# Kernel tuning notes

Hardware: AMD Instinct MI355X
Metric: run time of the kernel (lower is better)

## Reference

```python
import jax, jax.numpy as jnp
import numpy as np

B, P, O, C = 64, 8732, 32, 81
IMG = 224.0
THRESH = 0.5
NEG_POS = 3.0
ALPHA = 1.0


def cxcy_to_xy(b):
    return jnp.concatenate([b[..., :2] - b[..., 2:] / 2, b[..., :2] + b[..., 2:] / 2], -1)


def xy_to_cxcy(b):
    return jnp.concatenate([(b[..., :2] + b[..., 2:]) / 2, b[..., 2:] - b[..., :2]], -1)


def coco_to_xy(b):  # [x, y, w, h] -> [xmin, ymin, xmax, ymax]
    return jnp.concatenate([b[..., :2], b[..., :2] + b[..., 2:]], -1)


def cxcy_to_gcxgcy(cxcy, priors):  # SSD offset encoding, variances 10 / 5
    g_cxcy = (cxcy[..., :2] - priors[..., :2]) / (priors[..., 2:] / 10.0)
    g_wh = jnp.log(cxcy[..., 2:] / priors[..., 2:]) * 5.0
    return jnp.concatenate([g_cxcy, g_wh], -1)


def pairwise_iou(a, b):  # a: [O,4] xy, b: [P,4] xy -> [O,P]
    lt = jnp.maximum(a[:, None, :2], b[None, :, :2])
    rb = jnp.minimum(a[:, None, 2:], b[None, :, 2:])
    wh = jnp.clip(rb - lt, 0.0)
    inter = wh[..., 0] * wh[..., 1]
    area_a = (a[:, 2] - a[:, 0]) * (a[:, 3] - a[:, 1])
    area_b = (b[:, 2] - b[:, 0]) * (b[:, 3] - b[:, 1])
    return inter / (area_a[:, None] + area_b[None, :] - inter)


def setup_inputs() -> dict:
    key = jax.random.key(0)
    k1, k2, k3, k4, k5, k6, k7 = jax.random.split(key, 7)
    pred_locs = jax.random.normal(k1, (B, P, 4), dtype=jnp.float32)
    pred_scores = jax.random.normal(k2, (B, P, C), dtype=jnp.float32)
    # COCO-format gt boxes [x, y, w, h] in pixel coords, guaranteed inside image
    xy = jax.random.uniform(k3, (B, O, 2), minval=0.0, maxval=IMG * 0.55)
    wh = jax.random.uniform(k4, (B, O, 2), minval=8.0, maxval=IMG * 0.4)
    gt_boxes = jnp.concatenate([xy, wh], -1)
    gt_labels = jax.random.randint(k5, (B, O), 1, C)  # foreground labels 1..C-1
    p_cxcy = jax.random.uniform(k6, (P, 2), minval=0.05, maxval=0.95)
    p_wh = jax.random.uniform(k7, (P, 2), minval=0.05, maxval=0.5)
    priors_cxcy = jnp.concatenate([p_cxcy, p_wh], -1)
    return {"pred_locs": pred_locs, "pred_scores": pred_scores,
            "gt_boxes": gt_boxes, "gt_labels": gt_labels,
            "priors_cxcy": priors_cxcy}


def reference(pred_locs, pred_scores, gt_boxes, gt_labels, priors_cxcy):
    priors_xy = cxcy_to_xy(priors_cxcy)

    def match(boxes_coco, labels):  # one image: [O,4] coco, [O] int
        boxes_xy = coco_to_xy(boxes_coco) / IMG  # normalize to [0,1]
        ov = pairwise_iou(boxes_xy, priors_xy)  # [O, P]
        overlap_for_prior = ov.max(axis=0)       # [P]
        object_for_prior = ov.argmax(axis=0)     # [P]
        prior_for_object = ov.argmax(axis=1)     # [O]
        # force each object to claim its best prior
        object_for_prior = object_for_prior.at[prior_for_object].set(jnp.arange(O))
        overlap_for_prior = overlap_for_prior.at[prior_for_object].set(1.0)
        label_for_prior = labels[object_for_prior]
        label_for_prior = jnp.where(overlap_for_prior < THRESH, 0, label_for_prior)
        true_locs = cxcy_to_gcxgcy(xy_to_cxcy(boxes_xy[object_for_prior]), priors_cxcy)
        return true_locs, label_for_prior

    true_locs, true_classes = jax.vmap(match)(gt_boxes, gt_labels)  # [B,P,4], [B,P]

    positive = true_classes != 0          # [B, P]
    n_pos = positive.sum(axis=1)          # [B]
    n_pos_cl = jnp.maximum(n_pos, 1).astype(jnp.float32)
    n_hard_neg = NEG_POS * n_pos_cl

    # SmoothL1 (beta=1), mean over positive prior coords
    diff = jnp.abs(pred_locs - true_locs)
    sl1 = jnp.where(diff < 1.0, 0.5 * diff * diff, diff - 0.5)  # [B,P,4]
    total_pos = n_pos.sum()
    loc_loss = jnp.where(
        total_pos > 0,
        jnp.where(positive[..., None], sl1, 0.0).sum()
        / jnp.maximum(total_pos * 4, 1).astype(jnp.float32),
        0.0,
    )

    # per-prior cross entropy
    logp = jax.nn.log_softmax(pred_scores, axis=-1)
    ce = -jnp.take_along_axis(logp, true_classes[..., None], axis=-1)[..., 0]  # [B,P]

    conf_pos_sum = jnp.where(positive, ce, 0.0).sum()
    ce_neg = jnp.where(positive, 0.0, ce)
    ce_neg_sorted = -jnp.sort(-ce_neg, axis=1)  # descending per image
    ranks = jnp.arange(P)[None, :]
    hard = ranks < n_hard_neg[:, None]
    conf_hard_neg_sum = jnp.where(hard, ce_neg_sorted, 0.0).sum()

    conf_loss = (conf_hard_neg_sum + conf_pos_sum) / n_pos_cl.sum()
    return conf_loss + ALPHA * loc_loss
```

## Files before the change

### kernel.cpp

```cpp
#include <hip/hip_runtime.h>
#include <cstdint>
#include <cstddef>

#define BB 64
#define PP 8732
#define OO 32
#define CC 81
#define NR 64
#define NB3 137
#define NQ 4
#define QP 2183

__global__ __launch_bounds__(1024) void k_prep(
    const float* __restrict__ gt_boxes,
    const float4* __restrict__ priors,
    unsigned long long* __restrict__ part,
    int* __restrict__ done)
{
    int q = blockIdx.x, b = blockIdx.y, t = threadIdx.x;
    if (q == 0 && b == 0 && t == 0) *done = 0;
    int o = t >> 5, s = t & 31;
    __shared__ float4 s_pr[1024];
    const float* g = gt_boxes + ((size_t)b * OO + o) * 4;
    float x1 = g[0] / 224.0f, y1 = g[1] / 224.0f;
    float x2 = (g[0] + g[2]) / 224.0f, y2 = (g[1] + g[3]) / 224.0f;
    float area = (x2 - x1) * (y2 - y1);
    float best = -1.0f; int bp = 0;
    int p0 = q * QP;
    for (int base = 0; base < QP; base += 1024) {
        int idx = base + t;
        if (idx < QP) s_pr[t] = priors[p0 + idx];
        __syncthreads();
        int lim = QP - base; if (lim > 1024) lim = 1024;
        for (int j = s; j < lim; j += 128) {
            float iou4[4]; int jj4[4];
            #pragma unroll
            for (int u = 0; u < 4; ++u) {
                int jj = j + 32 * u;
                jj4[u] = jj;
                if (jj < lim) {
                    float4 pr = s_pr[jj];
                    float px1 = pr.x - pr.z * 0.5f, py1 = pr.y - pr.w * 0.5f;
                    float px2 = pr.x + pr.z * 0.5f, py2 = pr.y + pr.w * 0.5f;
                    float parea = (px2 - px1) * (py2 - py1);
                    float lx = fmaxf(x1, px1), ly = fmaxf(y1, py1);
                    float rx = fminf(x2, px2), ry = fminf(y2, py2);
                    float w = fmaxf(rx - lx, 0.0f), h = fmaxf(ry - ly, 0.0f);
                    float inter = w * h;
                    iou4[u] = inter / (area + parea - inter);
                } else iou4[u] = -2.0f;
            }
            #pragma unroll
            for (int u = 0; u < 4; ++u)
                if (iou4[u] > best) { best = iou4[u]; bp = p0 + base + jj4[u]; }
        }
        __syncthreads();
    }
    unsigned long long v = ((unsigned long long)__float_as_uint(best) << 32)
                         | (unsigned long long)(0xFFFFFFFFu - (unsigned)bp);
    #pragma unroll
    for (int sh = 16; sh >= 1; sh >>= 1) {
        unsigned long long u = __shfl_xor(v, sh, 32);
        if (u > v) v = u;
    }
    if (s == 0) part[((size_t)b * NQ + q) * OO + o] = v;
}

__global__ __launch_bounds__(256) void k_ce(
    const float* __restrict__ scores,
    const float4* __restrict__ pred_locs,
    const float* __restrict__ gt_boxes,
    const int* __restrict__ gt_labels,
    const float4* __restrict__ priors,
    const unsigned long long* __restrict__ part,
    float* __restrict__ ceneg,
    float* __restrict__ pp_posce, float* __restrict__ pp_sl1,
    int* __restrict__ pp_np)
{
    int b = blockIdx.y, tid = threadIdx.x;
    int row0 = blockIdx.x * NR;
    int nrows = PP - row0; if (nrows > NR) nrows = NR;

    __shared__ float sv[NR * CC];
    __shared__ float4 s_pr[NR];
    __shared__ float bx1[OO], by1[OO], bx2[OO], by2[OO], bar[OO];
    __shared__ int s_lab[OO];
    __shared__ int s_pfo[OO];
    __shared__ int s_force[NR];
    __shared__ float s_cn[NR];
    __shared__ float s_posce, s_sl1;
    __shared__ int s_np;

    if (tid == 0) { s_posce = 0.f; s_sl1 = 0.f; s_np = 0; }
    if (tid < OO) {
        const float* g = gt_boxes + ((size_t)b * OO + tid) * 4;
        float x1 = g[0] / 224.0f, y1 = g[1] / 224.0f;
        float x2 = (g[0] + g[2]) / 224.0f, y2 = (g[1] + g[3]) / 224.0f;
        bx1[tid] = x1; by1[tid] = y1; bx2[tid] = x2; by2[tid] = y2;
        bar[tid] = (x2 - x1) * (y2 - y1);
        s_lab[tid] = gt_labels[b * OO + tid];
        const unsigned long long* pb = part + (size_t)b * NQ * OO + tid;
        unsigned long long m = pb[0];
        #pragma unroll
        for (int qq = 1; qq < NQ; ++qq) {
            unsigned long long v = pb[qq * OO];
            if (v > m) m = v;
        }
        s_pfo[tid] = (int)(0xFFFFFFFFu - (unsigned)(m & 0xFFFFFFFFull));
    }
    if (tid < NR) {
        s_force[tid] = -1;
        if (row0 + tid < PP) s_pr[tid] = priors[row0 + tid];
    }
    __syncthreads();
    if (tid == 0) {
        #pragma unroll
        for (int o = 0; o < OO; ++o) {
            int rp = s_pfo[o] - row0;
            if (rp >= 0 && rp < nrows) s_force[rp] = o;
        }
    }
    {
        const float4* src4 = (const float4*)(scores + ((size_t)b * PP + row0) * CC);
        int nvec = nrows * CC / 4;
        float4* dst = (float4*)sv;
        for (int i = tid; i < nvec; i += 256) dst[i] = src4[i];
    }
    __syncthreads();

    int g = tid >> 4, lane = tid & 15;
    #pragma unroll
    for (int j = 0; j < 4; ++j) {
        int r = g + 16 * j;
        if (r < nrows) {
            float4 pq = s_pr[r];
            float px1 = pq.x - pq.z * 0.5f, py1 = pq.y - pq.w * 0.5f;
            float px2 = pq.x + pq.z * 0.5f, py2 = pq.y + pq.w * 0.5f;
            float parea = (px2 - px1) * (py2 - py1);
            float bi; int bo;
            {
                int o1 = lane, o2 = lane + 16;
                float lx = fmaxf(bx1[o1], px1), ly = fmaxf(by1[o1], py1);
                float rx = fminf(bx2[o1], px2), ry = fminf(by2[o1], py2);
                float w1 = fmaxf(rx - lx, 0.0f), h1 = fmaxf(ry - ly, 0.0f);
                float in1 = w1 * h1;
                float i1 = in1 / (bar[o1] + parea - in1);
                lx = fmaxf(bx1[o2], px1); ly = fmaxf(by1[o2], py1);
                rx = fminf(bx2[o2], px2); ry = fminf(by2[o2], py2);
                float w2 = fmaxf(rx - lx, 0.0f), h2 = fmaxf(ry - ly, 0.0f);
                float in2 = w2 * h2;
                float i2 = in2 / (bar[o2] + parea - in2);
                bi = i1; bo = o1;
                if (i2 > bi) { bi = i2; bo = o2; }
                unsigned long long pk = ((unsigned long long)__float_as_uint(bi) << 32)
                                      | (unsigned long long)(0xFFFFFFFFu - (unsigned)bo);
                #pragma unroll
                for (int s = 8; s >= 1; s >>= 1) {
                    unsigned long long u = __shfl_xor(pk, s, 16);
                    if (u > pk) pk = u;
                }
                bi = __uint_as_float((unsigned)(pk >> 32));
                bo = (int)(0xFFFFFFFFu - (unsigned)(pk & 0xFFFFFFFFull));
            }
            int fo = s_force[r];
            int lab, ob;
            if (fo >= 0) { ob = fo; lab = s_lab[fo]; }
            else         { ob = bo; lab = (bi < 0.5f) ? 0 : s_lab[bo]; }
            float se = 0.f, xl = 0.f;
            #pragma unroll
            for (int k = 0; k < 6; ++k) {
                int c = lane + 16 * k;
                if (c < CC) {
                    float vv = sv[r * CC + c];
                    se += __expf(vv);
                    if (c == lab) xl = vv;
                }
            }
            #pragma unroll
            for (int s = 8; s >= 1; s >>= 1) {
                se += __shfl_xor(se, s, 16);
                xl += __shfl_xor(xl, s, 16);
            }
            if (lane == 0) {
                float ce = fmaxf(__logf(se) - xl, 0.0f);
                float cn = ce;
                if (lab != 0) {
                    cn = 0.f;
                    float4 pl = pred_locs[(size_t)b * PP + row0 + r];
                    float x1 = bx1[ob], y1 = by1[ob], x2 = bx2[ob], y2 = by2[ob];
                    float cx = (x1 + x2) * 0.5f, cy = (y1 + y2) * 0.5f;
                    float w = x2 - x1, h = y2 - y1;
                    float tx = (cx - pq.x) / (pq.z / 10.0f);
                    float ty = (cy - pq.y) / (pq.w / 10.0f);
                    float tw = __logf(w / pq.z) * 5.0f;
                    float th = __logf(h / pq.w) * 5.0f;
                    float d0 = fabsf(pl.x - tx), d1 = fabsf(pl.y - ty);
                    float d2 = fabsf(pl.z - tw), d3 = fabsf(pl.w - th);
                    float sl = (d0 < 1.f ? 0.5f * d0 * d0 : d0 - 0.5f)
                             + (d1 < 1.f ? 0.5f * d1 * d1 : d1 - 0.5f)
                             + (d2 < 1.f ? 0.5f * d2 * d2 : d2 - 0.5f)
                             + (d3 < 1.f ? 0.5f * d3 * d3 : d3 - 0.5f);
                    atomicAdd(&s_posce, ce);
                    atomicAdd(&s_sl1, sl);
                    atomicAdd(&s_np, 1);
                }
                s_cn[r] = cn;
            }
        }
    }
    __syncthreads();
    if (tid < nrows) ceneg[(size_t)b * PP + row0 + tid] = s_cn[tid];
    if (tid == 0) {
        int slot = b * NB3 + blockIdx.x;
        pp_posce[slot] = s_posce;
        pp_sl1[slot]   = s_sl1;
        pp_np[slot]    = s_np;
    }
}

__global__ __launch_bounds__(512) void k_topk(
    const float* __restrict__ ceneg,
    const float* __restrict__ pp_posce, const float* __restrict__ pp_sl1,
    const int* __restrict__ pp_np,
    float* __restrict__ hard, float* __restrict__ posce_b,
    float* __restrict__ sl1_b, int* __restrict__ n_pos,
    int* __restrict__ done, float* __restrict__ out)
{
    int b = blockIdx.x, tid = threadIdx.x;
    __shared__ float4 sv4[PP / 4];
    __shared__ int hist[8][256];
    __shared__ int hsum[256];
    __shared__ int s_i[8];
    __shared__ float s_f[8], s_f2[8];
    __shared__ int s_bcast;
    __shared__ unsigned s_sel;
    __shared__ int s_krem;
    __shared__ int s_last;
    float pc = 0.f, sl = 0.f; int np = 0;
    for (int i = tid; i < NB3; i += 512) {
        pc += pp_posce[b * NB3 + i];
        sl += pp_sl1[b * NB3 + i];
        np += pp_np[b * NB3 + i];
    }
    #pragma unroll
    for (int s = 32; s >= 1; s >>= 1) {
        pc += __shfl_xor(pc, s, 64);
        sl += __shfl_xor(sl, s, 64);
        np += __shfl_xor(np, s, 64);
    }
    int wid = tid >> 6;
    if ((tid & 63) == 0) { s_i[wid] = np; s_f[wid] = pc; s_f2[wid] = sl; }
    const float4* src = (const float4*)(ceneg + (size_t)b * PP);
    for (int i = tid; i < PP / 4; i += 512) sv4[i] = src[i];
    __syncthreads();
    if (tid == 0) {
        int n = 0; float fp = 0.f, fs = 0.f;
        #pragma unroll
        for (int k = 0; k < 8; ++k) { n += s_i[k]; fp += s_f[k]; fs += s_f2[k]; }
        n_pos[b] = n; posce_b[b] = fp; sl1_b[b] = fs;
        s_bcast = n;
        int K0 = 3 * (n > 1 ? n : 1);
        if (K0 > PP) K0 = PP;
        s_sel = 0u; s_krem = K0;
    }
    __syncthreads();
    np = s_bcast;
    int K = 3 * (np > 1 ? np : 1);
    if (K > PP) K = PP;
    #pragma unroll
    for (int s = 24; s >= 0; s -= 8) {
        for (int i = tid; i < 8 * 256; i += 512) ((int*)hist)[i] = 0;
        __syncthreads();
        unsigned pref = s_sel; int krem = s_krem;
        int hs = s + 8;
        unsigned prefhi = (hs >= 32) ? 0u : (pref >> (hs & 31));
        for (int i = tid; i < PP / 4; i += 512) {
            float4 q = sv4[i];
            float vals[4] = {q.x, q.y, q.z, q.w};
            #pragma unroll
            for (int c4 = 0; c4 < 4; ++c4) {
                unsigned bts = __float_as_uint(vals[c4]);
                bool ok = (hs >= 32) || ((bts >> (hs & 31)) == prefhi);
                if (ok) atomicAdd(&hist[wid][(bts >> s) & 255], 1);
            }
        }
        __syncthreads();
        if (tid < 256) {
            int t = 0;
            #pragma unroll
            for (int k = 0; k < 8; ++k) t += hist[k][tid];
            hsum[tid] = t;
        }
        __syncthreads();
        if (tid < 64) {
            int ln = tid;
            int cum = 0;
            for (int c = 3; c >= 0; --c) {
                int h = hsum[c * 64 + ln];
                int suff = h;
                #pragma unroll
                for (int off = 1; off < 64; off <<= 1) {
                    int t = __shfl_down(suff, off);
                    if (ln + off < 64) suff += t;
                }
                int ctot = __shfl(suff, 0);
                if (cum + ctot >= krem) {
                    unsigned long long m = __ballot(cum + suff >= krem);
                    int l = 63 - __builtin_clzll(m);
                    int suffl = __shfl(suff, l);
                    int hl = __shfl(h, l);
                    if (ln == 0) {
                        s_sel = pref | ((unsigned)(c * 64 + l) << s);
                        s_krem = krem - (cum + suffl - hl);
                    }
                    break;
                }
                cum += ctot;
            }
        }
        __syncthreads();
    }
    float vk = __uint_as_float(s_sel);
    float sm = 0.f; int cg = 0;
    for (int i = tid; i < PP / 4; i += 512) {
        float4 q = sv4[i];
        if (q.x > vk) { sm += q.x; cg++; }
        if (q.y > vk) { sm += q.y; cg++; }
        if (q.z > vk) { sm += q.z; cg++; }
        if (q.w > vk) { sm += q.w; cg++; }
    }
    #pragma unroll
    for (int s = 32; s >= 1; s >>= 1) {
        sm += __shfl_xor(sm, s, 64);
        cg += __shfl_xor(cg, s, 64);
    }
    if ((tid & 63) == 0) { s_f[wid] = sm; s_i[wid] = cg; }
    __syncthreads();
    if (tid == 0) {
        float S = 0.f; int CG = 0;
        #pragma unroll
        for (int k = 0; k < 8; ++k) { S += s_f[k]; CG += s_i[k]; }
        hard[b] = S + (float)(K - CG) * vk;
    }
    __threadfence();
    if (tid == 0) s_last = (atomicAdd(done, 1) == BB - 1) ? 1 : 0;
    __syncthreads();
    if (s_last) {
        __threadfence();
        if (tid < 64) {
            int t = tid;
            int np2 = n_pos[t];
            float h2 = hard[t], pc2 = posce_b[t], sl2 = sl1_b[t];
            float cl = (float)(np2 > 1 ? np2 : 1);
            int tp = np2; float hs2 = h2; float cls = cl;
            #pragma unroll
            for (int sft = 32; sft >= 1; sft >>= 1) {
                tp  += __shfl_xor(tp, sft, 64);
                hs2 += __shfl_xor(hs2, sft, 64);
                cls += __shfl_xor(cls, sft, 64);
                pc2 += __shfl_xor(pc2, sft, 64);
                sl2 += __shfl_xor(sl2, sft, 64);
            }
            if (t == 0) {
                float conf = (hs2 + pc2) / cls;
                float loc = 0.f;
                if (tp > 0) {
                    int den = tp * 4; if (den < 1) den = 1;
                    loc = sl2 / (float)den;
                }
                out[0] = conf + loc;
            }
        }
    }
}

extern "C" void kernel_launch(void* const* d_in, const int* in_sizes, int n_in,
                              void* d_out, int out_size, void* d_ws, size_t ws_size,
                              hipStream_t stream)
{
    const float* pred_locs   = (const float*)d_in[0];
    const float* pred_scores = (const float*)d_in[1];
    const float* gt_boxes    = (const float*)d_in[2];
    const int*   gt_labels   = (const int*)d_in[3];
    const float* priors      = (const float*)d_in[4];

    char* ws = (char*)d_ws;
    const size_t npf = (size_t)BB * PP;
    size_t off = 0;
    float* ceneg = (float*)(ws + off); off += 4 * npf;
    unsigned long long* part = (unsigned long long*)(ws + off); off += 8 * (size_t)BB * NQ * OO;
    float* pp_posce = (float*)(ws + off); off += 4 * (size_t)BB * NB3;
    float* pp_sl1   = (float*)(ws + off); off += 4 * (size_t)BB * NB3;
    int*   pp_np    = (int*)  (ws + off); off += 4 * (size_t)BB * NB3;
    float* posce_b  = (float*)(ws + off); off += 4 * BB;
    float* sl1_b    = (float*)(ws + off); off += 4 * BB;
    int*   n_pos    = (int*)  (ws + off); off += 4 * BB;
    float* hard     = (float*)(ws + off); off += 4 * BB;
    int*   done     = (int*)  (ws + off); off += 4;

    dim3 gP(NQ, BB);
    k_prep<<<gP, 1024, 0, stream>>>(gt_boxes, (const float4*)priors, part, done);

    dim3 gB(NB3, BB);
    k_ce<<<gB, 256, 0, stream>>>(pred_scores, (const float4*)pred_locs, gt_boxes, gt_labels,
                                 (const float4*)priors, part, ceneg,
                                 pp_posce, pp_sl1, pp_np);

    k_topk<<<BB, 512, 0, stream>>>(ceneg, pp_posce, pp_sl1, pp_np,
                                   hard, posce_b, sl1_b, n_pos, done, (float*)d_out);
}
```

Baseline: 339.2 us.

## Restructure CE kernel to one thread per prior row with larger tiles

The CE/matching kernel now gives each thread a whole prior row. It uses 128-row tiles and 128-thread blocks instead of 16-lane groups per row over 64-row tiles. Each thread computes IoU against all 32 GT boxes serially and sums the softmax with four accumulators, which removes the cross-lane shuffle reductions. The shared-memory staging loop issues four float4 loads before storing them, to keep more loads in flight, and the per-row output staging buffer is dropped. In exchange, each block uses about twice the LDS with fewer waves, which may reduce occupancy and latency hiding on this memory-bound stage.

New measurement: 333.4 us. Within noise of the previous version (-1.7%).

```diff
diff --git a/kernel.cpp b/kernel.cpp
--- a/kernel.cpp
+++ b/kernel.cpp
@@ -6,10 +6,10 @@
 #define PP 8732
 #define OO 32
 #define CC 81
-#define NR 64
-#define NB3 137
 #define NQ 4
 #define QP 2183
+#define NR4 128
+#define NB4 69
 
 __global__ __launch_bounds__(1024) void k_prep(
     const float* __restrict__ gt_boxes,
@@ -66,7 +66,7 @@
     if (s == 0) part[((size_t)b * NQ + q) * OO + o] = v;
 }
 
-__global__ __launch_bounds__(256) void k_ce(
+__global__ __launch_bounds__(128) void k_ce(
     const float* __restrict__ scores,
     const float4* __restrict__ pred_locs,
     const float* __restrict__ gt_boxes,
@@ -78,16 +78,14 @@
     int* __restrict__ pp_np)
 {
     int b = blockIdx.y, tid = threadIdx.x;
-    int row0 = blockIdx.x * NR;
-    int nrows = PP - row0; if (nrows > NR) nrows = NR;
-
-    __shared__ float sv[NR * CC];
-    __shared__ float4 s_pr[NR];
+    int row0 = blockIdx.x * NR4;
+    int nrows = PP - row0; if (nrows > NR4) nrows = NR4;
+
+    __shared__ float sv[NR4 * CC];
     __shared__ float bx1[OO], by1[OO], bx2[OO], by2[OO], bar[OO];
     __shared__ int s_lab[OO];
     __shared__ int s_pfo[OO];
-    __shared__ int s_force[NR];
-    __shared__ float s_cn[NR];
+    __shared__ int s_force[NR4];
     __shared__ float s_posce, s_sl1;
     __shared__ int s_np;
 
@@ -108,10 +106,7 @@
         }
         s_pfo[tid] = (int)(0xFFFFFFFFu - (unsigned)(m & 0xFFFFFFFFull));
     }
-    if (tid < NR) {
-        s_force[tid] = -1;
-        if (row0 + tid < PP) s_pr[tid] = priors[row0 + tid];
-    }
+    s_force[tid] = -1;
     __syncthreads();
     if (tid == 0) {
         #pragma unroll
@@ -122,96 +117,82 @@
     }
     {
         const float4* src4 = (const float4*)(scores + ((size_t)b * PP + row0) * CC);
+        float4* dst = (float4*)sv;
         int nvec = nrows * CC / 4;
-        float4* dst = (float4*)sv;
-        for (int i = tid; i < nvec; i += 256) dst[i] = src4[i];
-    }
-    __syncthreads();
-
-    int g = tid >> 4, lane = tid & 15;
-    #pragma unroll
-    for (int j = 0; j < 4; ++j) {
-        int r = g + 16 * j;
-        if (r < nrows) {
-            float4 pq = s_pr[r];
-            float px1 = pq.x - pq.z * 0.5f, py1 = pq.y - pq.w * 0.5f;
-            float px2 = pq.x + pq.z * 0.5f, py2 = pq.y + pq.w * 0.5f;
-            float parea = (px2 - px1) * (py2 - py1);
-            float bi; int bo;
-            {
-                int o1 = lane, o2 = lane + 16;
-                float lx = fmaxf(bx1[o1], px1), ly = fmaxf(by1[o1], py1);
-                float rx = fminf(bx2[o1], px2), ry = fminf(by2[o1], py2);
-                float w1 = fmaxf(rx - lx, 0.0f), h1 = fmaxf(ry - ly, 0.0f);
-                float in1 = w1 * h1;
-                float i1 = in1 / (bar[o1] + parea - in1);
-                lx = fmaxf(bx1[o2], px1); ly = fmaxf(by1[o2], py1);
-                rx = fminf(bx2[o2], px2); ry = fminf(by2[o2], py2);
-                float w2 = fmaxf(rx - lx, 0.0f), h2 = fmaxf(ry - ly, 0.0f);
-                float in2 = w2 * h2;
-                float i2 = in2 / (bar[o2] + parea - in2);
-                bi = i1; bo = o1;
-                if (i2 > bi) { bi = i2; bo = o2; }
-                unsigned long long pk = ((unsigned long long)__float_as_uint(bi) << 32)
-                                      | (unsigned long long)(0xFFFFFFFFu - (unsigned)bo);
-                #pragma unroll
-                for (int s = 8; s >= 1; s >>= 1) {
-                    unsigned long long u = __shfl_xor(pk, s, 16);
-                    if (u > pk) pk = u;
-                }
-                bi = __uint_as_float((unsigned)(pk >> 32));
-                bo = (int)(0xFFFFFFFFu - (unsigned)(pk & 0xFFFFFFFFull));
-            }
-            int fo = s_force[r];
-            int lab, ob;
-            if (fo >= 0) { ob = fo; lab = s_lab[fo]; }
-            else         { ob = bo; lab = (bi < 0.5f) ? 0 : s_lab[bo]; }
-            float se = 0.f, xl = 0.f;
-            #pragma unroll
-            for (int k = 0; k < 6; ++k) {
-                int c = lane + 16 * k;
-                if (c < CC) {
-                    float vv = sv[r * CC + c];
-                    se += __expf(vv);
-                    if (c == lab) xl = vv;
-                }
-            }
-            #pragma unroll
-            for (int s = 8; s >= 1; s >>= 1) {
-                se += __shfl_xor(se, s, 16);
-                xl += __shfl_xor(xl, s, 16);
-            }
-            if (lane == 0) {
-                float ce = fmaxf(__logf(se) - xl, 0.0f);
-                float cn = ce;
-                if (lab != 0) {
-                    cn = 0.f;
-                    float4 pl = pred_locs[(size_t)b * PP + row0 + r];
-                    float x1 = bx1[ob], y1 = by1[ob], x2 = bx2[ob], y2 = by2[ob];
-                    float cx = (x1 + x2) * 0.5f, cy = (y1 + y2) * 0.5f;
-                    float w = x2 - x1, h = y2 - y1;
-                    float tx = (cx - pq.x) / (pq.z / 10.0f);
-                    float ty = (cy - pq.y) / (pq.w / 10.0f);
-                    float tw = __logf(w / pq.z) * 5.0f;
-                    float th = __logf(h / pq.w) * 5.0f;
-                    float d0 = fabsf(pl.x - tx), d1 = fabsf(pl.y - ty);
-                    float d2 = fabsf(pl.z - tw), d3 = fabsf(pl.w - th);
-                    float sl = (d0 < 1.f ? 0.5f * d0 * d0 : d0 - 0.5f)
-                             + (d1 < 1.f ? 0.5f * d1 * d1 : d1 - 0.5f)
-                             + (d2 < 1.f ? 0.5f * d2 * d2 : d2 - 0.5f)
-                             + (d3 < 1.f ? 0.5f * d3 * d3 : d3 - 0.5f);
-                    atomicAdd(&s_posce, ce);
-                    atomicAdd(&s_sl1, sl);
-                    atomicAdd(&s_np, 1);
-                }
-                s_cn[r] = cn;
-            }
-        }
-    }
-    __syncthreads();
-    if (tid < nrows) ceneg[(size_t)b * PP + row0 + tid] = s_cn[tid];
+        for (int base = 0; base < nvec; base += 512) {
+            int i0 = base + tid, i1 = i0 + 128, i2 = i0 + 256, i3 = i0 + 384;
+            bool v0 = i0 < nvec, v1 = i1 < nvec, v2 = i2 < nvec, v3 = i3 < nvec;
+            float4 t0, t1, t2, t3;
+            if (v0) t0 = src4[i0];
+            if (v1) t1 = src4[i1];
+            if (v2) t2 = src4[i2];
+            if (v3) t3 = src4[i3];
+            if (v0) dst[i0] = t0;
+            if (v1) dst[i1] = t1;
+            if (v2) dst[i2] = t2;
+            if (v3) dst[i3] = t3;
+        }
+    }
+    __syncthreads();
+
+    if (tid < nrows) {
+        int p = row0 + tid;
+        float4 pq = priors[p];
+        float px1 = pq.x - pq.z * 0.5f, py1 = pq.y - pq.w * 0.5f;
+        float px2 = pq.x + pq.z * 0.5f, py2 = pq.y + pq.w * 0.5f;
+        float parea = (px2 - px1) * (py2 - py1);
+        float bi = -1.0f; int bo = 0;
+        #pragma unroll
+        for (int o = 0; o < OO; ++o) {
+            float lx = fmaxf(bx1[o], px1), ly = fmaxf(by1[o], py1);
+            float rx = fminf(bx2[o], px2), ry = fminf(by2[o], py2);
+            float w = fmaxf(rx - lx, 0.0f), h = fmaxf(ry - ly, 0.0f);
+            float inter = w * h;
+            float iou = inter / (bar[o] + parea - inter);
+            if (iou > bi) { bi = iou; bo = o; }
+        }
+        int fo = s_force[tid];
+        int lab, ob;
+        if (fo >= 0) { ob = fo; lab = s_lab[fo]; }
+        else         { ob = bo; lab = (bi < 0.5f) ? 0 : s_lab[bo]; }
+        const float* row = sv + tid * CC;
+        float se0 = 0.f, se1 = 0.f, se2 = 0.f, se3 = 0.f;
+        #pragma unroll
+        for (int c = 0; c < 80; c += 4) {
+            se0 += __expf(row[c]);
+            se1 += __expf(row[c + 1]);
+            se2 += __expf(row[c + 2]);
+            se3 += __expf(row[c + 3]);
+        }
+        float se = (se0 + se1) + (se2 + se3) + __expf(row[80]);
+        float xl = row[lab];
+        float ce = fmaxf(__logf(se) - xl, 0.0f);
+        float cn = ce;
+        if (lab != 0) {
+            cn = 0.f;
+            float4 pl = pred_locs[(size_t)b * PP + p];
+            float x1 = bx1[ob], y1 = by1[ob], x2 = bx2[ob], y2 = by2[ob];
+            float cx = (x1 + x2) * 0.5f, cy = (y1 + y2) * 0.5f;
+            float w = x2 - x1, h = y2 - y1;
+            float tx = (cx - pq.x) / (pq.z / 10.0f);
+            float ty = (cy - pq.y) / (pq.w / 10.0f);
+            float tw = __logf(w / pq.z) * 5.0f;
+            float th = __logf(h / pq.w) * 5.0f;
+            float d0 = fabsf(pl.x - tx), d1 = fabsf(pl.y - ty);
+            float d2 = fabsf(pl.z - tw), d3 = fabsf(pl.w - th);
+            float sl = (d0 < 1.f ? 0.5f * d0 * d0 : d0 - 0.5f)
+                     + (d1 < 1.f ? 0.5f * d1 * d1 : d1 - 0.5f)
+                     + (d2 < 1.f ? 0.5f * d2 * d2 : d2 - 0.5f)
+                     + (d3 < 1.f ? 0.5f * d3 * d3 : d3 - 0.5f);
+            atomicAdd(&s_posce, ce);
+            atomicAdd(&s_sl1, sl);
+            atomicAdd(&s_np, 1);
+        }
+        ceneg[(size_t)b * PP + p] = cn;
+    }
+    __syncthreads();
     if (tid == 0) {
-        int slot = b * NB3 + blockIdx.x;
+        int slot = b * NB4 + blockIdx.x;
         pp_posce[slot] = s_posce;
         pp_sl1[slot]   = s_sl1;
         pp_np[slot]    = s_np;
@@ -237,10 +218,10 @@
     __shared__ int s_krem;
     __shared__ int s_last;
     float pc = 0.f, sl = 0.f; int np = 0;
-    for (int i = tid; i < NB3; i += 512) {
-        pc += pp_posce[b * NB3 + i];
-        sl += pp_sl1[b * NB3 + i];
-        np += pp_np[b * NB3 + i];
+    for (int i = tid; i < NB4; i += 512) {
+        pc += pp_posce[b * NB4 + i];
+        sl += pp_sl1[b * NB4 + i];
+        np += pp_np[b * NB4 + i];
     }
     #pragma unroll
     for (int s = 32; s >= 1; s >>= 1) {
@@ -389,9 +370,9 @@
     size_t off = 0;
     float* ceneg = (float*)(ws + off); off += 4 * npf;
     unsigned long long* part = (unsigned long long*)(ws + off); off += 8 * (size_t)BB * NQ * OO;
-    float* pp_posce = (float*)(ws + off); off += 4 * (size_t)BB * NB3;
-    float* pp_sl1   = (float*)(ws + off); off += 4 * (size_t)BB * NB3;
-    int*   pp_np    = (int*)  (ws + off); off += 4 * (size_t)BB * NB3;
+    float* pp_posce = (float*)(ws + off); off += 4 * (size_t)BB * NB4;
+    float* pp_sl1   = (float*)(ws + off); off += 4 * (size_t)BB * NB4;
+    int*   pp_np    = (int*)  (ws + off); off += 4 * (size_t)BB * NB4;
     float* posce_b  = (float*)(ws + off); off += 4 * BB;
     float* sl1_b    = (float*)(ws + off); off += 4 * BB;
     int*   n_pos    = (int*)  (ws + off); off += 4 * BB;
@@ -401,8 +382,8 @@
     dim3 gP(NQ, BB);
     k_prep<<<gP, 1024, 0, stream>>>(gt_boxes, (const float4*)priors, part, done);
 
-    dim3 gB(NB3, BB);
-    k_ce<<<gB, 256, 0, stream>>>(pred_scores, (const float4*)pred_locs, gt_boxes, gt_labels,
+    dim3 gB(NB4, BB);
+    k_ce<<<gB, 128, 0, stream>>>(pred_scores, (const float4*)pred_locs, gt_boxes, gt_labels,
                                  (const float4*)priors, part, ceneg,
                                  pp_posce, pp_sl1, pp_np);
 
```
